# Kernel optimization log

Measured on AMD Instinct MI355X. Metric: run time of the kernel, lower is better.

The kernel has to match this reference:

```python
import jax, jax.numpy as jnp
import numpy as np

N_HEAD = 8  # config.n_head

def _ln(x, g, b):
    # eqx.nn.LayerNorm, eps=1e-5
    m = x.mean(-1, keepdims=True)
    v = ((x - m) ** 2).mean(-1, keepdims=True)
    return (x - m) / jnp.sqrt(v + 1e-5) * g + b

def _lin(x, w, b):
    # eqx.nn.Linear: weight [out, in]
    return x @ w.T + b

def _heads(t):
    B, T, C = t.shape
    return t.reshape(B, T, N_HEAD, C // N_HEAD).transpose(0, 2, 1, 3)  # [B,H,T,d]

def _merge(t):
    B, H, T, d = t.shape
    return t.transpose(0, 2, 1, 3).reshape(B, T, H * d)

def setup_inputs() -> dict:
    key = jax.random.key(0)
    B, T1, T2, C, INNER, NIN = 4, 4096, 4096, 512, 2048, 2
    ks = jax.random.split(key, 16)
    w = lambda k, *s: 0.02 * jax.random.normal(k, s, dtype=jnp.float32)
    return {
        'x': jax.random.normal(ks[0], (B, T1, C), dtype=jnp.float32),
        'ys': jax.random.normal(ks[1], (NIN, B, T2, C), dtype=jnp.float32),
        'ln1_g': jnp.ones((C,)), 'ln1_b': jnp.zeros((C,)),
        'ln2_g': jnp.ones((NIN, C)), 'ln2_b': jnp.zeros((NIN, C)),
        'ln3_g': jnp.ones((C,)), 'ln3_b': jnp.zeros((C,)),
        'ln4_g': jnp.ones((C,)), 'ln4_b': jnp.zeros((C,)),
        'ln5_g': jnp.ones((C,)), 'ln5_b': jnp.zeros((C,)),
        'ca_wq': w(ks[2], C, C), 'ca_bq': jnp.zeros((C,)),
        'ca_wk': w(ks[3], NIN, C, C), 'ca_bk': jnp.zeros((NIN, C)),
        'ca_wv': w(ks[4], NIN, C, C), 'ca_bv': jnp.zeros((NIN, C)),
        'ca_wo': w(ks[5], C, C), 'ca_bo': jnp.zeros((C,)),
        'sa_wq': w(ks[6], C, C), 'sa_bq': jnp.zeros((C,)),
        'sa_wk': w(ks[7], C, C), 'sa_bk': jnp.zeros((C,)),
        'sa_wv': w(ks[8], C, C), 'sa_bv': jnp.zeros((C,)),
        'sa_wo': w(ks[9], C, C), 'sa_bo': jnp.zeros((C,)),
        'ffn1_w1': w(ks[10], INNER, C), 'ffn1_b1': jnp.zeros((INNER,)),
        'ffn1_w2': w(ks[11], C, INNER), 'ffn1_b2': jnp.zeros((C,)),
        'ffn2_w1': w(ks[12], INNER, C), 'ffn2_b1': jnp.zeros((INNER,)),
        'ffn2_w2': w(ks[13], C, INNER), 'ffn2_b2': jnp.zeros((C,)),
    }

def reference(x, ys, ln1_g, ln1_b, ln2_g, ln2_b, ln3_g, ln3_b, ln4_g, ln4_b, ln5_g, ln5_b,
              ca_wq, ca_bq, ca_wk, ca_bk, ca_wv, ca_bv, ca_wo, ca_bo,
              sa_wq, sa_bq, sa_wk, sa_bk, sa_wv, sa_bv, sa_wo, sa_bo,
              ffn1_w1, ffn1_b1, ffn1_w2, ffn1_b2, ffn2_w1, ffn2_b1, ffn2_w2, ffn2_b2):
    n_inputs = ys.shape[0]
    # ---- linear cross attention ----
    xn = _ln(x, ln1_g, ln1_b)
    q = jax.nn.softmax(_heads(_lin(xn, ca_wq, ca_bq)), axis=-1)  # [B,H,T1,d]
    out = q
    for i in range(n_inputs):  # small fixed branch count
        yn = _ln(ys[i], ln2_g[i], ln2_b[i])
        k = jax.nn.softmax(_heads(_lin(yn, ca_wk[i], ca_bk[i])), axis=-1)  # [B,H,T2,d]
        v = _heads(_lin(yn, ca_wv[i], ca_bv[i]))
        k_sum = k.sum(axis=-2, keepdims=True)                       # [B,H,1,d]
        D_inv = 1.0 / ((q * k_sum).sum(axis=-1, keepdims=True) + 1e-8)
        ctx = jnp.einsum('bhnd,bhnv->bhdv', k, v)                   # [B,H,d,d]
        out = out + jnp.einsum('bhqd,bhdv->bhqv', q, ctx) * D_inv
    x = x + _lin(_merge(out), ca_wo, ca_bo)
    # ---- FFN 1 ----
    xn = _ln(x, ln3_g, ln3_b)
    x = x + _lin(jax.nn.gelu(_lin(xn, ffn1_w1, ffn1_b1)), ffn1_w2, ffn1_b2)
    # ---- linear self attention (attn_type='l1') ----
    xn = _ln(x, ln4_g, ln4_b)
    q = jax.nn.softmax(_heads(_lin(xn, sa_wq, sa_bq)), axis=-1)
    k = jax.nn.softmax(_heads(_lin(xn, sa_wk, sa_bk)), axis=-1)
    v = _heads(_lin(xn, sa_wv, sa_bv))
    k_sum = k.sum(axis=-2, keepdims=True)
    D_inv = 1.0 / (q * k_sum).sum(axis=-1, keepdims=True)  # no eps in 'l1' branch
    ctx = jnp.einsum('bhnd,bhnv->bhdv', k, v)
    sa = jnp.einsum('bhqd,bhdv->bhqv', q, ctx) * D_inv + q
    x = x + _lin(_merge(sa), sa_wo, sa_bo)
    # ---- FFN 2 ----
    xn = _ln(x, ln5_g, ln5_b)
    x = x + _lin(jax.nn.gelu(_lin(xn, ffn2_w1, ffn2_b1)), ffn2_w2, ffn2_b2)
    return x
```

## Files before the change

kernel.cpp:

```cpp
#include <hip/hip_runtime.h>
#include <hip/hip_bf16.h>
#include <math.h>
#include <stdint.h>

typedef unsigned short u16;
typedef __attribute__((ext_vector_type(8))) short bh8;
typedef __attribute__((ext_vector_type(4))) float fx4;

#define DEV static __device__ __forceinline__

DEV float bf2f(u16 u){ union{unsigned u; float f;} v; v.u = ((unsigned)u)<<16; return v.f; }
DEV u16 f2bf(float f){ union{float f; unsigned u;} v; v.f = f;
  return (u16)((v.u + 0x7fffu + ((v.u>>16)&1u))>>16); }

DEV void async16(const u16* g, u16* l){
  __builtin_amdgcn_global_load_lds((__attribute__((address_space(1))) void*)(uintptr_t)g,
                                   (__attribute__((address_space(3))) void*)l, 16, 0, 0);
}

DEV float gelu_fast(float x){
  float u = 0.7978845608f*(x + 0.044715f*x*x*x);
  float e = __expf(-2.f*fabsf(u));
  float t = __fdividef(1.f - e, 1.f + e);
  t = copysignf(t, u);
  return 0.5f*x*(1.f + t);
}

struct WDesc { const float* src[14]; int off[14]; };
__global__ __launch_bounds__(256) void convw_kernel(WDesc d, u16* __restrict__ dst){
  int i = blockIdx.x*256 + threadIdx.x;
  int s = 0;
  #pragma unroll
  for(int j=1;j<14;j++) if(i >= d.off[j]) s = j;
  dst[i] = f2bf(d.src[s][i - d.off[s]]);
}

DEV float wsum64(float s){
  s += __shfl_xor(s,1,64);  s += __shfl_xor(s,2,64);  s += __shfl_xor(s,4,64);
  s += __shfl_xor(s,8,64);  s += __shfl_xor(s,16,64); s += __shfl_xor(s,32,64);
  return s;
}
__global__ __launch_bounds__(256) void ln_kernel(const float* __restrict__ x,
    const float* __restrict__ g, const float* __restrict__ bta, u16* __restrict__ out){
  int row  = blockIdx.x*4 + (threadIdx.x>>6);
  int lane = threadIdx.x & 63;
  const float4* xr = (const float4*)(x + (size_t)row*512) + lane*2;
  float4 a = xr[0], c = xr[1];
  float s = a.x+a.y+a.z+a.w + c.x+c.y+c.z+c.w;
  float mean = wsum64(s) * (1.f/512.f);
  float d0=a.x-mean,d1=a.y-mean,d2=a.z-mean,d3=a.w-mean;
  float d4=c.x-mean,d5=c.y-mean,d6=c.z-mean,d7=c.w-mean;
  float sv = d0*d0+d1*d1+d2*d2+d3*d3+d4*d4+d5*d5+d6*d6+d7*d7;
  float rstd = rsqrtf(wsum64(sv)*(1.f/512.f) + 1e-5f);
  const float4* gr = (const float4*)g   + lane*2;
  const float4* br = (const float4*)bta + lane*2;
  float4 g0=gr[0], g1=gr[1], b0=br[0], b1=br[1];
  bh8 o;
  o[0]=(short)f2bf(d0*rstd*g0.x+b0.x); o[1]=(short)f2bf(d1*rstd*g0.y+b0.y);
  o[2]=(short)f2bf(d2*rstd*g0.z+b0.z); o[3]=(short)f2bf(d3*rstd*g0.w+b0.w);
  o[4]=(short)f2bf(d4*rstd*g1.x+b1.x); o[5]=(short)f2bf(d5*rstd*g1.y+b1.y);
  o[6]=(short)f2bf(d6*rstd*g1.z+b1.z); o[7]=(short)f2bf(d7*rstd*g1.w+b1.w);
  *(bh8*)(out + (size_t)row*512 + lane*8) = o;
}

DEV void xcd_map(int nbx, int& bn, int& bm){
  int lid = blockIdx.y*nbx + blockIdx.x;
  int per = (nbx*128)>>3;
  int sid = (lid&7)*per + (lid>>3);
  bn = sid % nbx; bm = sid / nbx;
}

struct SubD { const float* bias; u16* out; float* ksum; int mode; };
struct Subs3 { SubD s[3]; };
__global__ __launch_bounds__(256) void gemm_qkv(const u16* __restrict__ A,
    const u16* __restrict__ W, Subs3 subs, int K){
  __shared__ __align__(16) u16 lsA[128*32];
  __shared__ __align__(16) u16 lsB[128*32];
  const int tid = threadIdx.x, lane = tid&63, w = tid>>6;
  const int quad = lane>>4, l15 = lane&15;
  int bn, bm; xcd_map(gridDim.x, bn, bm);
  const int wm = w&1, wn = w>>1;
  fx4 acc[4][4];
  #pragma unroll
  for(int i=0;i<4;i++)
    #pragma unroll
    for(int j=0;j<4;j++) acc[i][j] = (fx4){0.f,0.f,0.f,0.f};
  const u16* Ab = A + (size_t)bm*128*K;
  const u16* Wb = W + (size_t)bn*128*K;
  const int srow = w*32 + (lane>>2);
  const int scol = (lane&3)*8;
  for(int k0=0;k0<K;k0+=32){
    __syncthreads();
    async16(Ab + (size_t)srow*K      + k0 + scol, &lsA[(w*32   )*32]);
    async16(Ab + (size_t)(srow+16)*K + k0 + scol, &lsA[(w*32+16)*32]);
    async16(Wb + (size_t)srow*K      + k0 + scol, &lsB[(w*32   )*32]);
    async16(Wb + (size_t)(srow+16)*K + k0 + scol, &lsB[(w*32+16)*32]);
    __syncthreads();
    bh8 af[4], bfx[4];
    #pragma unroll
    for(int t=0;t<4;t++){
      af[t]  = *(const bh8*)&lsA[(wm*64+t*16+l15)*32 + quad*8];
      bfx[t] = *(const bh8*)&lsB[(wn*64+t*16+l15)*32 + quad*8];
    }
    #pragma unroll
    for(int mt=0;mt<4;mt++)
      #pragma unroll
      for(int nt=0;nt<4;nt++)
        acc[mt][nt] = __builtin_amdgcn_mfma_f32_16x16x32_bf16(af[mt], bfx[nt], acc[mt][nt], 0,0,0);
  }
  const SubD sub = subs.s[bn>>2];
  const int colw = (bn&3)*128 + wn*64;
  float bcol[4];
  #pragma unroll
  for(int nt=0;nt<4;nt++) bcol[nt] = sub.bias[colw + nt*16 + l15];

  if(sub.mode==1){
    float ksacc[4] = {0.f,0.f,0.f,0.f};
    #pragma unroll
    for(int mt=0;mt<4;mt++)
      #pragma unroll
      for(int r=0;r<4;r++){
        float v0=acc[mt][0][r]+bcol[0], v1=acc[mt][1][r]+bcol[1];
        float v2=acc[mt][2][r]+bcol[2], v3=acc[mt][3][r]+bcol[3];
        float mx = fmaxf(fmaxf(v0,v1),fmaxf(v2,v3));
        mx = fmaxf(mx,__shfl_xor(mx,1,64)); mx = fmaxf(mx,__shfl_xor(mx,2,64));
        mx = fmaxf(mx,__shfl_xor(mx,4,64)); mx = fmaxf(mx,__shfl_xor(mx,8,64));
        float e0=__expf(v0-mx), e1=__expf(v1-mx), e2=__expf(v2-mx), e3=__expf(v3-mx);
        float s = e0+e1+e2+e3;
        s += __shfl_xor(s,1,64); s += __shfl_xor(s,2,64);
        s += __shfl_xor(s,4,64); s += __shfl_xor(s,8,64);
        float inv = __fdividef(1.f, s);
        e0*=inv; e1*=inv; e2*=inv; e3*=inv;
        ksacc[0]+=e0; ksacc[1]+=e1; ksacc[2]+=e2; ksacc[3]+=e3;
        int row = bm*128 + wm*64 + mt*16 + quad*4 + r;
        size_t rb = (size_t)row*512;
        sub.out[rb+colw+ 0+l15]=f2bf(e0); sub.out[rb+colw+16+l15]=f2bf(e1);
        sub.out[rb+colw+32+l15]=f2bf(e2); sub.out[rb+colw+48+l15]=f2bf(e3);
      }
    if(sub.ksum){
      int b = bm>>5;
      #pragma unroll
      for(int nt=0;nt<4;nt++){
        float s = ksacc[nt];
        s += __shfl_xor(s,16,64); s += __shfl_xor(s,32,64);
        if(quad==0) atomicAdd(&sub.ksum[b*512 + colw + nt*16 + l15], s);
      }
    }
  } else {
    #pragma unroll
    for(int mt=0;mt<4;mt++)
      #pragma unroll
      for(int r=0;r<4;r++){
        int row = bm*128 + wm*64 + mt*16 + quad*4 + r;
        size_t rb = (size_t)row*512;
        #pragma unroll
        for(int nt=0;nt<4;nt++)
          sub.out[rb + colw + nt*16 + l15] = f2bf(acc[mt][nt][r] + bcol[nt]);
      }
  }
}

template<int EPI>
__global__ __launch_bounds__(256) void gemm_bt(const u16* __restrict__ A,
    const u16* __restrict__ W, const float* __restrict__ bias,
    const float* __restrict__ res, void* __restrict__ out, int N, int K){
  __shared__ __align__(16) u16 lsA[128*32];
  __shared__ __align__(16) u16 lsB[128*32];
  const int tid = threadIdx.x, lane = tid&63, w = tid>>6;
  const int quad = lane>>4, l15 = lane&15;
  int bn, bm; xcd_map(gridDim.x, bn, bm);
  const int wm = w&1, wn = w>>1;
  fx4 acc[4][4];
  #pragma unroll
  for(int i=0;i<4;i++)
    #pragma unroll
    for(int j=0;j<4;j++) acc[i][j] = (fx4){0.f,0.f,0.f,0.f};
  const u16* Ab = A + (size_t)bm*128*K;
  const u16* Wb = W + (size_t)bn*128*K;
  const int srow = w*32 + (lane>>2);
  const int scol = (lane&3)*8;
  for(int k0=0;k0<K;k0+=32){
    __syncthreads();
    async16(Ab + (size_t)srow*K      + k0 + scol, &lsA[(w*32   )*32]);
    async16(Ab + (size_t)(srow+16)*K + k0 + scol, &lsA[(w*32+16)*32]);
    async16(Wb + (size_t)srow*K      + k0 + scol, &lsB[(w*32   )*32]);
    async16(Wb + (size_t)(srow+16)*K + k0 + scol, &lsB[(w*32+16)*32]);
    __syncthreads();
    bh8 af[4], bfx[4];
    #pragma unroll
    for(int t=0;t<4;t++){
      af[t]  = *(const bh8*)&lsA[(wm*64+t*16+l15)*32 + quad*8];
      bfx[t] = *(const bh8*)&lsB[(wn*64+t*16+l15)*32 + quad*8];
    }
    #pragma unroll
    for(int mt=0;mt<4;mt++)
      #pragma unroll
      for(int nt=0;nt<4;nt++)
        acc[mt][nt] = __builtin_amdgcn_mfma_f32_16x16x32_bf16(af[mt], bfx[nt], acc[mt][nt], 0,0,0);
  }
  const int colbase = bn*128 + wn*64;
  float bcol[4];
  #pragma unroll
  for(int nt=0;nt<4;nt++) bcol[nt] = bias[colbase + nt*16 + l15];

  if(EPI==3){
    float* of = (float*)out;
    #pragma unroll
    for(int mt=0;mt<4;mt++)
      #pragma unroll
      for(int r=0;r<4;r++){
        int row = bm*128 + wm*64 + mt*16 + quad*4 + r;
        size_t rb = (size_t)row*N;
        #pragma unroll
        for(int nt=0;nt<4;nt++){
          int col = colbase + nt*16 + l15;
          of[rb+col] = res[rb+col] + acc[mt][nt][r] + bcol[nt];
        }
      }
  } else {
    u16* ob = (u16*)out;
    #pragma unroll
    for(int mt=0;mt<4;mt++)
      #pragma unroll
      for(int r=0;r<4;r++){
        int row = bm*128 + wm*64 + mt*16 + quad*4 + r;
        size_t rb = (size_t)row*N;
        #pragma unroll
        for(int nt=0;nt<4;nt++)
          ob[rb + colbase + nt*16 + l15] = f2bf(gelu_fast(acc[mt][nt][r] + bcol[nt]));
      }
  }
}

__global__ __launch_bounds__(256) void ctx_kernel(const u16* __restrict__ kb,
    const u16* __restrict__ vb, float* __restrict__ ctx){
  __shared__ __align__(16) u16 lk[64*72];
  __shared__ __align__(16) u16 lv[64*72];
  const int tid=threadIdx.x, lane=tid&63, w=tid>>6, quad=lane>>4, l15=lane&15;
  const int bh = blockIdx.x, h = bh&7;
  const size_t rowbase = ((size_t)(bh>>3))*4096 + (size_t)blockIdx.y*512;
  const int mt0=(w&1)*32, nt0=(w>>1)*32;
  fx4 acc[2][2];
  #pragma unroll
  for(int i=0;i<2;i++)
    #pragma unroll
    for(int j=0;j<2;j++) acc[i][j] = (fx4){0.f,0.f,0.f,0.f};
  const int tl = tid>>2, part = tid&3;
  for(int it=0; it<8; it++){
    __syncthreads();
    {
      size_t gro = (rowbase + it*64 + tl)*512 + h*64 + part*16;
      bh8 k0 = *(const bh8*)(kb + gro); bh8 k1 = *(const bh8*)(kb + gro + 8);
      bh8 v0 = *(const bh8*)(vb + gro); bh8 v1 = *(const bh8*)(vb + gro + 8);
      #pragma unroll
      for(int j=0;j<8;j++){
        lk[(part*16+j  )*72 + tl] = (u16)k0[j];
        lk[(part*16+8+j)*72 + tl] = (u16)k1[j];
        lv[(part*16+j  )*72 + tl] = (u16)v0[j];
        lv[(part*16+8+j)*72 + tl] = (u16)v1[j];
      }
    }
    __syncthreads();
    #pragma unroll
    for(int ks=0;ks<2;ks++){
      bh8 a0 = *(const bh8*)&lk[(mt0    +l15)*72 + ks*32 + quad*8];
      bh8 a1 = *(const bh8*)&lk[(mt0+16 +l15)*72 + ks*32 + quad*8];
      bh8 b0 = *(const bh8*)&lv[(nt0    +l15)*72 + ks*32 + quad*8];
      bh8 b1 = *(const bh8*)&lv[(nt0+16 +l15)*72 + ks*32 + quad*8];
      acc[0][0] = __builtin_amdgcn_mfma_f32_16x16x32_bf16(a0,b0,acc[0][0],0,0,0);
      acc[0][1] = __builtin_amdgcn_mfma_f32_16x16x32_bf16(a0,b1,acc[0][1],0,0,0);
      acc[1][0] = __builtin_amdgcn_mfma_f32_16x16x32_bf16(a1,b0,acc[1][0],0,0,0);
      acc[1][1] = __builtin_amdgcn_mfma_f32_16x16x32_bf16(a1,b1,acc[1][1],0,0,0);
    }
  }
  float* cb = ctx + (size_t)bh*4096;
  #pragma unroll
  for(int mi=0;mi<2;mi++)
    #pragma unroll
    for(int ni=0;ni<2;ni++)
      #pragma unroll
      for(int r=0;r<4;r++){
        int d1 = mt0 + mi*16 + quad*4 + r;
        int d2 = nt0 + ni*16 + l15;
        atomicAdd(&cb[d1*64 + d2], acc[mi][ni][r]);
      }
}

__global__ __launch_bounds__(256) void dinv_kernel(const u16* __restrict__ q,
    const float* __restrict__ ksum, float* __restrict__ dinv, int n_in, float eps){
  int gidx = blockIdx.x*256 + threadIdx.x;
  int token = gidx>>3, h = gidx&7, b = token>>12;
  const u16* qr = q + (size_t)token*512 + h*64;
  float qv[64];
  #pragma unroll
  for(int d=0;d<64;d++) qv[d] = bf2f(qr[d]);
  for(int i=0;i<n_in;i++){
    const float* ks = ksum + i*2048 + b*512 + h*64;
    float s = 0.f;
    #pragma unroll
    for(int d=0;d<64;d++) s += qv[d]*ks[d];
    dinv[(size_t)i*131072 + gidx] = __fdividef(1.f, s + eps);
  }
}

template<int NIN>
__global__ __launch_bounds__(256) void apply_kernel(const u16* __restrict__ q,
    const float* __restrict__ ctx, const float* __restrict__ dinv, u16* __restrict__ out){
  __shared__ __align__(16) u16 lctx[(NIN+1)*64*72];
  const int tid=threadIdx.x, lane=tid&63, w=tid>>6, quad=lane>>4, l15=lane&15;
  const int bh = blockIdx.x, b=bh>>3, h=bh&7;
  {
    int base = tid*16;
    int d1 = base>>6, d2b = base&63;
    #pragma unroll
    for(int s=0;s<=NIN;s++){
      u16* dst = &lctx[s*64*72];
      if(s<NIN){
        const float* sp = ctx + ((size_t)s*32 + bh)*4096 + base;
        #pragma unroll
        for(int j=0;j<16;j++) dst[(d2b+j)*72 + d1] = f2bf(sp[j]);
      } else {
        #pragma unroll
        for(int j=0;j<16;j++) dst[(d2b+j)*72 + d1] = ((d2b+j)==d1) ? (u16)0x3f80 : (u16)0;
      }
    }
  }
  __syncthreads();
  bh8 bfr[NIN+1][4][2];
  #pragma unroll
  for(int s=0;s<=NIN;s++)
    #pragma unroll
    for(int nt=0;nt<4;nt++)
      #pragma unroll
      for(int ks=0;ks<2;ks++)
        bfr[s][nt][ks] = *(const bh8*)&lctx[s*64*72 + (nt*16+l15)*72 + ks*32 + quad*8];
  const size_t tb0 = (size_t)b*4096 + (size_t)blockIdx.y*256 + w*64;
  for(int g=0;g<4;g++){
    size_t tb = tb0 + g*16;
    const u16* qr = q + (tb + l15)*512 + h*64;
    bh8 a0 = *(const bh8*)(qr + quad*8);
    bh8 a1 = *(const bh8*)(qr + 32 + quad*8);
    fx4 outv[4];
    #pragma unroll
    for(int nt=0;nt<4;nt++) outv[nt] = (fx4){0.f,0.f,0.f,0.f};
    #pragma unroll
    for(int s=0;s<=NIN;s++){
      fx4 c[4];
      #pragma unroll
      for(int nt=0;nt<4;nt++){
        c[nt] = (fx4){0.f,0.f,0.f,0.f};
        c[nt] = __builtin_amdgcn_mfma_f32_16x16x32_bf16(a0, bfr[s][nt][0], c[nt], 0,0,0);
        c[nt] = __builtin_amdgcn_mfma_f32_16x16x32_bf16(a1, bfr[s][nt][1], c[nt], 0,0,0);
      }
      float dv[4];
      #pragma unroll
      for(int r=0;r<4;r++)
        dv[r] = (s==NIN) ? 1.f : dinv[(size_t)s*131072 + (tb+quad*4+r)*8 + h];
      #pragma unroll
      for(int nt=0;nt<4;nt++)
        #pragma unroll
        for(int r=0;r<4;r++) outv[nt][r] += c[nt][r]*dv[r];
    }
    #pragma unroll
    for(int nt=0;nt<4;nt++)
      #pragma unroll
      for(int r=0;r<4;r++)
        out[(tb+quad*4+r)*512 + h*64 + nt*16 + l15] = f2bf(outv[nt][r]);
  }
}

extern "C" void kernel_launch(void* const* d_in, const int* in_sizes, int n_in,
                              void* d_out, int out_size, void* d_ws, size_t ws_size,
                              hipStream_t stream){
  const float* x_in =(const float*)d_in[0];
  const float* ys   =(const float*)d_in[1];
  const float* ln1g =(const float*)d_in[2],  *ln1b=(const float*)d_in[3];
  const float* ln2g =(const float*)d_in[4],  *ln2b=(const float*)d_in[5];
  const float* ln3g =(const float*)d_in[6],  *ln3b=(const float*)d_in[7];
  const float* ln4g =(const float*)d_in[8],  *ln4b=(const float*)d_in[9];
  const float* ln5g =(const float*)d_in[10], *ln5b=(const float*)d_in[11];
  const float* ca_wq=(const float*)d_in[12], *ca_bq=(const float*)d_in[13];
  const float* ca_wk=(const float*)d_in[14], *ca_bk=(const float*)d_in[15];
  const float* ca_wv=(const float*)d_in[16], *ca_bv=(const float*)d_in[17];
  const float* ca_wo=(const float*)d_in[18], *ca_bo=(const float*)d_in[19];
  const float* sa_wq=(const float*)d_in[20], *sa_bq=(const float*)d_in[21];
  const float* sa_wk=(const float*)d_in[22], *sa_bk=(const float*)d_in[23];
  const float* sa_wv=(const float*)d_in[24], *sa_bv=(const float*)d_in[25];
  const float* sa_wo=(const float*)d_in[26], *sa_bo=(const float*)d_in[27];
  const float* f1w1 =(const float*)d_in[28], *f1b1=(const float*)d_in[29];
  const float* f1w2 =(const float*)d_in[30], *f1b2=(const float*)d_in[31];
  const float* f2w1 =(const float*)d_in[32], *f2b1=(const float*)d_in[33];
  const float* f2w2 =(const float*)d_in[34], *f2b2=(const float*)d_in[35];

  char* p = (char*)d_ws;
  u16*   WBF = (u16*)p;    p += 13631488;
  float* XW  = (float*)p;  p += 33554432;
  u16*   XN  = (u16*)p;    p += 16777216;
  u16*   QB  = (u16*)p;    p += 16777216;
  u16*   KB  = (u16*)p;    p += 16777216;
  u16*   VB  = (u16*)p;    p += 16777216;
  u16*   HB  = (u16*)p;    p += 67108864;
  float* SM  = (float*)p;  p += 1597440;
  float* DINV= (float*)p;  p += 1048576;
  float* CTXC = SM;
  float* CTXS = SM + 262144;
  float* KSC  = SM + 393216;
  float* KSS  = SM + 397312;
  u16*   OUTB = HB;

  WDesc wd;
  const float* wsrc[14] = {ca_wq, ca_wk, ca_wv, ca_wk+262144, ca_wv+262144, ca_wo,
                           sa_wq, sa_wk, sa_wv, sa_wo, f1w1, f1w2, f2w1, f2w2};
  const int    woff[14] = {0, 262144, 524288, 786432, 1048576, 1310720,
                           1572864, 1835008, 2097152, 2359296,
                           2621440, 3670016, 4718592, 5767168};
  for(int i=0;i<14;i++){ wd.src[i]=wsrc[i]; wd.off[i]=woff[i]; }
  convw_kernel<<<26624,256,0,stream>>>(wd, WBF);
  hipMemsetAsync(SM, 0, 399360*sizeof(float), stream);

  SubD zsub = {nullptr,nullptr,nullptr,0};

  ln_kernel<<<4096,256,0,stream>>>(x_in, ln1g, ln1b, XN);
  { Subs3 s = {{ {ca_bq, QB, nullptr, 1}, zsub, zsub }};
    gemm_qkv<<<dim3(4,128),256,0,stream>>>(XN, WBF+0, s, 512); }
  for(int i=0;i<2;i++){
    ln_kernel<<<4096,256,0,stream>>>(ys + (size_t)i*16384*512, ln2g+i*512, ln2b+i*512, XN);
    { Subs3 s = {{ {ca_bk+i*512, KB, KSC+i*2048, 1}, {ca_bv+i*512, VB, nullptr, 0}, zsub }};
      gemm_qkv<<<dim3(8,128),256,0,stream>>>(XN, WBF+262144+i*524288, s, 512); }
    ctx_kernel<<<dim3(32,8),256,0,stream>>>(KB, VB, CTXC + (size_t)i*131072);
  }
  dinv_kernel<<<512,256,0,stream>>>(QB, KSC, DINV, 2, 1e-8f);
  apply_kernel<2><<<dim3(32,16),256,0,stream>>>(QB, CTXC, DINV, OUTB);
  gemm_bt<3><<<dim3(4,128),256,0,stream>>>(OUTB, WBF+1310720, ca_bo, x_in, XW, 512, 512);

  ln_kernel<<<4096,256,0,stream>>>(XW, ln3g, ln3b, XN);
  gemm_bt<2><<<dim3(16,128),256,0,stream>>>(XN, WBF+2621440, f1b1, nullptr, HB, 2048, 512);
  gemm_bt<3><<<dim3(4,128),256,0,stream>>>(HB, WBF+3670016, f1b2, XW, XW, 512, 2048);

  ln_kernel<<<4096,256,0,stream>>>(XW, ln4g, ln4b, XN);
  { Subs3 s = {{ {sa_bq, QB, nullptr, 1}, {sa_bk, KB, KSS, 1}, {sa_bv, VB, nullptr, 0} }};
    gemm_qkv<<<dim3(12,128),256,0,stream>>>(XN, WBF+1572864, s, 512); }
  ctx_kernel<<<dim3(32,8),256,0,stream>>>(KB, VB, CTXS);
  dinv_kernel<<<512,256,0,stream>>>(QB, KSS, DINV, 1, 0.f);
  apply_kernel<1><<<dim3(32,16),256,0,stream>>>(QB, CTXS, DINV, OUTB);
  gemm_bt<3><<<dim3(4,128),256,0,stream>>>(OUTB, WBF+2359296, sa_bo, XW, XW, 512, 512);

  ln_kernel<<<4096,256,0,stream>>>(XW, ln5g, ln5b, XN);
  gemm_bt<2><<<dim3(16,128),256,0,stream>>>(XN, WBF+4718592, f2b1, nullptr, HB, 2048, 512);
  gemm_bt<3><<<dim3(4,128),256,0,stream>>>(HB, WBF+5767168, f2b2, XW, (float*)d_out, 512, 2048);
}
```

Baseline: 803.8 us.

## Swizzle LDS tile columns in GEMM k-loop and drop XCD block remapping

The shared GEMM k-loop moves into a macro. Global-to-LDS loads now place each 16-byte chunk at a column XOR-swizzled by row bits, and the MFMA fragment reads use the matching swizzled offset. The aim is to cut LDS bank conflicts on the ds_read of fragments. The change also drops the XCD-aware block index remapping in favour of plain blockIdx, which alters L2 locality across the chiplets.

```diff
diff --git a/kernel.cpp b/kernel.cpp
--- a/kernel.cpp
+++ b/kernel.cpp
@@ -63,12 +63,29 @@
   *(bh8*)(out + (size_t)row*512 + lane*8) = o;
 }
 
-DEV void xcd_map(int nbx, int& bn, int& bm){
-  int lid = blockIdx.y*nbx + blockIdx.x;
-  int per = (nbx*128)>>3;
-  int sid = (lid&7)*per + (lid>>3);
-  bn = sid % nbx; bm = sid / nbx;
-}
+#define GEMM_KLOOP(Ab, Wb, K)                                                        \
+  const int srow = w*32 + (lane>>2);                                                 \
+  const int scol = (((lane&3) ^ ((srow>>1)&3)) * 8);                                 \
+  const int rsw  = ((l15>>1)&3) ^ quad;                \
+  for(int k0=0;k0<K;k0+=32){                                                         \
+    __syncthreads();                                                                 \
+    async16(Ab + (size_t)srow*K      + k0 + scol, &lsA[(w*32   )*32]);               \
+    async16(Ab + (size_t)(srow+16)*K + k0 + scol, &lsA[(w*32+16)*32]);               \
+    async16(Wb + (size_t)srow*K      + k0 + scol, &lsB[(w*32   )*32]);               \
+    async16(Wb + (size_t)(srow+16)*K + k0 + scol, &lsB[(w*32+16)*32]);               \
+    __syncthreads();                                                                 \
+    bh8 af[4], bfx[4];                                                               \
+    _Pragma("unroll")                                                                \
+    for(int t=0;t<4;t++){                                                            \
+      af[t]  = *(const bh8*)&lsA[(wm*64+t*16+l15)*32 + rsw*8];                       \
+      bfx[t] = *(const bh8*)&lsB[(wn*64+t*16+l15)*32 + rsw*8];                       \
+    }                                                                                \
+    _Pragma("unroll")                                                                \
+    for(int mt=0;mt<4;mt++)                                                          \
+      _Pragma("unroll")                                                              \
+      for(int nt=0;nt<4;nt++)                                                        \
+        acc[mt][nt] = __builtin_amdgcn_mfma_f32_16x16x32_bf16(af[mt], bfx[nt], acc[mt][nt], 0,0,0); \
+  }
 
 struct SubD { const float* bias; u16* out; float* ksum; int mode; };
 struct Subs3 { SubD s[3]; };
@@ -78,7 +95,7 @@
   __shared__ __align__(16) u16 lsB[128*32];
   const int tid = threadIdx.x, lane = tid&63, w = tid>>6;
   const int quad = lane>>4, l15 = lane&15;
-  int bn, bm; xcd_map(gridDim.x, bn, bm);
+  const int bn = blockIdx.x, bm = blockIdx.y;
   const int wm = w&1, wn = w>>1;
   fx4 acc[4][4];
   #pragma unroll
@@ -87,27 +104,7 @@
     for(int j=0;j<4;j++) acc[i][j] = (fx4){0.f,0.f,0.f,0.f};
   const u16* Ab = A + (size_t)bm*128*K;
   const u16* Wb = W + (size_t)bn*128*K;
-  const int srow = w*32 + (lane>>2);
-  const int scol = (lane&3)*8;
-  for(int k0=0;k0<K;k0+=32){
-    __syncthreads();
-    async16(Ab + (size_t)srow*K      + k0 + scol, &lsA[(w*32   )*32]);
-    async16(Ab + (size_t)(srow+16)*K + k0 + scol, &lsA[(w*32+16)*32]);
-    async16(Wb + (size_t)srow*K      + k0 + scol, &lsB[(w*32   )*32]);
-    async16(Wb + (size_t)(srow+16)*K + k0 + scol, &lsB[(w*32+16)*32]);
-    __syncthreads();
-    bh8 af[4], bfx[4];
-    #pragma unroll
-    for(int t=0;t<4;t++){
-      af[t]  = *(const bh8*)&lsA[(wm*64+t*16+l15)*32 + quad*8];
-      bfx[t] = *(const bh8*)&lsB[(wn*64+t*16+l15)*32 + quad*8];
-    }
-    #pragma unroll
-    for(int mt=0;mt<4;mt++)
-      #pragma unroll
-      for(int nt=0;nt<4;nt++)
-        acc[mt][nt] = __builtin_amdgcn_mfma_f32_16x16x32_bf16(af[mt], bfx[nt], acc[mt][nt], 0,0,0);
-  }
+  GEMM_KLOOP(Ab, Wb, K)
   const SubD sub = subs.s[bn>>2];
   const int colw = (bn&3)*128 + wn*64;
   float bcol[4];
@@ -168,7 +165,7 @@
   __shared__ __align__(16) u16 lsB[128*32];
   const int tid = threadIdx.x, lane = tid&63, w = tid>>6;
   const int quad = lane>>4, l15 = lane&15;
-  int bn, bm; xcd_map(gridDim.x, bn, bm);
+  const int bn = blockIdx.x, bm = blockIdx.y;
   const int wm = w&1, wn = w>>1;
   fx4 acc[4][4];
   #pragma unroll
@@ -177,27 +174,7 @@
     for(int j=0;j<4;j++) acc[i][j] = (fx4){0.f,0.f,0.f,0.f};
   const u16* Ab = A + (size_t)bm*128*K;
   const u16* Wb = W + (size_t)bn*128*K;
-  const int srow = w*32 + (lane>>2);
-  const int scol = (lane&3)*8;
-  for(int k0=0;k0<K;k0+=32){
-    __syncthreads();
-    async16(Ab + (size_t)srow*K      + k0 + scol, &lsA[(w*32   )*32]);
-    async16(Ab + (size_t)(srow+16)*K + k0 + scol, &lsA[(w*32+16)*32]);
-    async16(Wb + (size_t)srow*K      + k0 + scol, &lsB[(w*32   )*32]);
-    async16(Wb + (size_t)(srow+16)*K + k0 + scol, &lsB[(w*32+16)*32]);
-    __syncthreads();
-    bh8 af[4], bfx[4];
-    #pragma unroll
-    for(int t=0;t<4;t++){
-      af[t]  = *(const bh8*)&lsA[(wm*64+t*16+l15)*32 + quad*8];
-      bfx[t] = *(const bh8*)&lsB[(wn*64+t*16+l15)*32 + quad*8];
-    }
-    #pragma unroll
-    for(int mt=0;mt<4;mt++)
-      #pragma unroll
-      for(int nt=0;nt<4;nt++)
-        acc[mt][nt] = __builtin_amdgcn_mfma_f32_16x16x32_bf16(af[mt], bfx[nt], acc[mt][nt], 0,0,0);
-  }
+  GEMM_KLOOP(Ab, Wb, K)
   const int colbase = bn*128 + wn*64;
   float bcol[4];
   #pragma unroll
```

Result: no change. 818.2 us (+1.8%).
